# Kernel tuning notes

Hardware: AMD Instinct MI355X
Metric: run time of the kernel (lower is better)

## Reference

```python
import jax, jax.numpy as jnp
import numpy as np

DIM = 256
N = 262144
LN_EPS = 1e-5


def setup_inputs() -> dict:
    key = jax.random.key(0)
    ks = jax.random.split(key, 16)
    d = DIM
    inp = {
        "x": jax.random.normal(ks[0], (N, d), dtype=jnp.float32),
        # main cell params (torch Linear stores weight as [out, in])
        "W_slow": jax.random.normal(ks[1], (d, d), dtype=jnp.float32) / np.sqrt(d),
        "V_slow": jax.random.normal(ks[2], (d, d), dtype=jnp.float32) * (0.1 / np.sqrt(d)),
        "gate_w": jax.random.normal(ks[3], (1, d), dtype=jnp.float32) / np.sqrt(d),
        "gate_b": jnp.zeros((1,), dtype=jnp.float32),
        # homeostatic core: Linear(4,16) -> LN(16) -> Tanh -> Linear(16,8) -> ReLU -> Linear(8,4) -> Sigmoid
        "sens1_w": jax.random.normal(ks[4], (16, 4), dtype=jnp.float32) * 0.5,
        "sens1_b": jnp.zeros((16,), dtype=jnp.float32),
        "ln_g": jnp.ones((16,), dtype=jnp.float32),
        "ln_b": jnp.zeros((16,), dtype=jnp.float32),
        "sens2_w": jax.random.normal(ks[5], (8, 16), dtype=jnp.float32) * 0.25,
        "sens2_b": jnp.zeros((8,), dtype=jnp.float32),
        "act_w": jax.random.normal(ks[6], (4, 8), dtype=jnp.float32) * 0.35,
        "act_b": jnp.zeros((4,), dtype=jnp.float32),
        # persistent Hebbian memory buffer
        "semantic_memory": jax.random.normal(ks[7], (d, d), dtype=jnp.float32) * 0.01,
    }
    return inp


def _homeostatic_controls(x, h_raw, w_norm, sens1_w, sens1_b, ln_g, ln_b,
                          sens2_w, sens2_b, act_w, act_b):
    # state vector: [surprise, excitation, fatigue, coherence]  -> [N, 4]
    surprise = jnp.abs(jnp.var(x, axis=1) - 0.5)          # unbiased=False variance
    excitation = jnp.mean(jnp.abs(h_raw), axis=1)
    fatigue = jnp.full_like(surprise, w_norm)
    coherence = jnp.full_like(surprise, 0.5)              # loss_val is None
    state = jnp.stack([surprise, excitation, fatigue, coherence], axis=1)
    z = state @ sens1_w.T + sens1_b                        # [N,16]
    mu = jnp.mean(z, axis=-1, keepdims=True)
    var = jnp.mean((z - mu) ** 2, axis=-1, keepdims=True)
    z = (z - mu) * jax.lax.rsqrt(var + LN_EPS) * ln_g + ln_b
    z = jnp.tanh(z)
    z = jax.nn.relu(z @ sens2_w.T + sens2_b)               # [N,8]
    controls = jax.nn.sigmoid(z @ act_w.T + act_b)         # [N,4]
    return controls


def reference(x, W_slow, V_slow, gate_w, gate_b,
              sens1_w, sens1_b, ln_g, ln_b, sens2_w, sens2_b, act_w, act_b,
              semantic_memory):
    # v = clamp(V_slow(x), -2, 2)
    v = jnp.clip(x @ V_slow.T, -2.0, 2.0)                  # [N, d]

    # homeostatic core (no_grad in torch)
    h_raw = x @ W_slow.T
    w_norm = jnp.linalg.norm(W_slow)
    controls = _homeostatic_controls(x, h_raw, w_norm, sens1_w, sens1_b,
                                     ln_g, ln_b, sens2_w, sens2_b, act_w, act_b)
    metabolic_rate = jnp.mean(controls[:, 0])
    gate_value = jnp.mean(controls[:, 2])

    gate = jax.nn.sigmoid(v @ gate_w.T + gate_b) * gate_value  # [N,1]
    output = jnp.clip(gate * v, -2.0, 2.0)

    # training-mode Hebbian memory update (no_grad in torch)
    batch = x.shape[0]
    hebb = (v.T @ x) / batch                               # [d, d]
    forget = jnp.mean(v ** 2, axis=0)[:, None] * semantic_memory
    delta = jnp.tanh(hebb - forget)
    mem = semantic_memory + delta * metabolic_rate * 0.1
    mem_norm = jnp.maximum(jnp.linalg.norm(mem), 1e-6)
    new_memory = mem / mem_norm * 0.5

    return output, new_memory
```

## Files before the change

### kernel.cpp

```cpp
#include <hip/hip_runtime.h>
#include <hip/hip_bf16.h>


#define NTOK 262144

typedef short s16x4 __attribute__((ext_vector_type(4)));
typedef short s16x8 __attribute__((ext_vector_type(8)));
typedef float f32x4 __attribute__((ext_vector_type(4)));
typedef unsigned int u32x4 __attribute__((ext_vector_type(4)));
typedef __bf16 bf16x8 __attribute__((ext_vector_type(8)));

static __device__ __forceinline__ float b2f(short s) {
  unsigned int u = ((unsigned int)(unsigned short)s) << 16;
  return __builtin_bit_cast(float, u);
}
static __device__ __forceinline__ short f2b(float f) {
  __hip_bfloat16 h = __float2bfloat16(f);
  return (short)__builtin_bit_cast(unsigned short, h);
}
static __device__ __forceinline__ float clip2(float f) {
  return fminf(2.f, fmaxf(-2.f, f));
}
static __device__ __forceinline__ unsigned int packu(short lo, short hi) {
  return (unsigned int)(unsigned short)lo | ((unsigned int)(unsigned short)hi << 16);
}
static __device__ __forceinline__ f32x4 mfma16(s16x8 a, s16x8 b, f32x4 c) {
  return __builtin_amdgcn_mfma_f32_16x16x32_bf16(
      __builtin_bit_cast(bf16x8, a), __builtin_bit_cast(bf16x8, b), c, 0, 0, 0);
}

__global__ __launch_bounds__(1024) void k_prep(const float* __restrict__ V,
                                               const float* __restrict__ W,
                                               short* __restrict__ Vf,
                                               short* __restrict__ Wf,
                                               float* __restrict__ scal) {
  int t = blockIdx.x * 1024 + threadIdx.x;
  int flat = t * 4;
  int col = flat >> 8, k0 = flat & 255;
  f32x4 v4 = *(const f32x4*)(V + flat);
  f32x4 w4 = *(const f32x4*)(W + flat);
  s16x4 vb, wb;
  float s = 0.f;
#pragma unroll
  for (int e = 0; e < 4; ++e) {
    vb[e] = f2b(v4[e]);
    wb[e] = f2b(w4[e]);
    s += w4[e] * w4[e];
  }
  int cb = col >> 4, lrr = col & 15;
  int ks = k0 >> 5, lgg = (k0 >> 3) & 3, j0 = k0 & 7;
  size_t g = (size_t)(((cb * 8 + ks) * 4 + lgg) * 16 + lrr) * 8 + j0;
  *(s16x4*)(Vf + g) = vb;
  *(s16x4*)(Wf + g) = wb;
#pragma unroll
  for (int d = 1; d < 64; d <<= 1) s += __shfl_xor(s, d);
  __shared__ float r[16];
  if ((threadIdx.x & 63) == 0) r[threadIdx.x >> 6] = s;
  __syncthreads();
  if (threadIdx.x == 0) {
    float tt = 0.f;
#pragma unroll
    for (int i = 0; i < 16; ++i) tt += r[i];
    atomicAdd(&scal[0], tt);
  }
}

__global__ __launch_bounds__(512) void k_main(
    const float* __restrict__ x, const short* __restrict__ Vf,
    const short* __restrict__ Wf, const float* __restrict__ gw,
    const float* __restrict__ gb, const float* __restrict__ s1w,
    const float* __restrict__ s1b, const float* __restrict__ lng,
    const float* __restrict__ lnb, const float* __restrict__ s2w,
    const float* __restrict__ s2b, const float* __restrict__ aw,
    const float* __restrict__ ab, short* __restrict__ v_out,
    float* __restrict__ g_out, float* __restrict__ scal) {
  __shared__ __align__(16) short xs[1024 * 8];
  __shared__ __align__(16) short vs[32 * 264];
  __shared__ float stat[4096];
  int tid = threadIdx.x;
  int lane = tid & 63, wid = tid >> 6;
  int lr = lane & 15, lg = lane >> 4;
  int np = tid >> 5, ic = tid & 31;
  int c0 = wid * 32;
  size_t n0 = (size_t)blockIdx.x * 1024;

#pragma unroll
  for (int q = 0; q < 4; ++q) stat[q * 512 + tid] = 0.f;

  float gw0 = gw[c0 + lr], gw1 = gw[c0 + 16 + lr];
  int sks = ic >> 2, slg = ic & 3;

  for (int nt = 0; nt < 32; ++nt) {
    int rbase = nt * 32;
    if (nt > 0) {
#pragma unroll
      for (int q = 0; q < 2; ++q) {
        int item = q * 512 + tid;
        int row = item >> 5, c8 = item & 31;
        *(s16x8*)(v_out + (n0 + rbase - 32 + row) * 256 + c8 * 8) =
            *(const s16x8*)(vs + row * 264 + c8 * 8);
      }
    }
    {
      const float* pa = x + (n0 + rbase + 2 * np) * 256 + ic * 8;
      f32x4 xa0 = *(const f32x4*)pa;
      f32x4 xa1 = *(const f32x4*)(pa + 4);
      f32x4 xb0 = *(const f32x4*)(pa + 256);
      f32x4 xb1 = *(const f32x4*)(pa + 260);
      s16x8 ca, cb;
      float sA = 0.f, qA = 0.f, sB = 0.f, qB = 0.f;
#pragma unroll
      for (int j = 0; j < 4; ++j) {
        sA += xa0[j] + xa1[j];
        qA += xa0[j] * xa0[j] + xa1[j] * xa1[j];
        sB += xb0[j] + xb1[j];
        qB += xb0[j] * xb0[j] + xb1[j] * xb1[j];
        ca[j] = f2b(xa0[j]); ca[4 + j] = f2b(xa1[j]);
        cb[j] = f2b(xb0[j]); cb[4 + j] = f2b(xb1[j]);
      }
      int rowa = 2 * np, rowb = 2 * np + 1;
      int sa = ((rowa >> 4) * 8 + sks) * 64 + ((slg * 16 + (rowa & 15)) ^ sks);
      int sb = ((rowb >> 4) * 8 + sks) * 64 + ((slg * 16 + (rowb & 15)) ^ sks);
      *(s16x8*)(xs + sa * 8) = ca;
      *(s16x8*)(xs + sb * 8) = cb;
#pragma unroll
      for (int d = 1; d < 32; d <<= 1) {
        sA += __shfl_xor(sA, d); qA += __shfl_xor(qA, d);
        sB += __shfl_xor(sB, d); qB += __shfl_xor(qB, d);
      }
      if (ic == 0) {
        stat[2048 + rbase + 2 * np] = sA;
        stat[3072 + rbase + 2 * np] = qA;
        stat[2048 + rbase + 2 * np + 1] = sB;
        stat[3072 + rbase + 2 * np + 1] = qB;
      }
    }
    __syncthreads();
    f32x4 av[2][2] = {}, ah[2][2] = {};
#pragma unroll
    for (int ks = 0; ks < 8; ++ks) {
      s16x8 a0 = *(const s16x8*)(xs + ((ks * 64) + (lane ^ ks)) * 8);
      s16x8 a1 = *(const s16x8*)(xs + (((8 + ks) * 64) + (lane ^ ks)) * 8);
      s16x8 bv0 = *(const s16x8*)(Vf + (size_t)(((wid * 2 + 0) * 8 + ks) * 64 + lane) * 8);
      s16x8 bv1 = *(const s16x8*)(Vf + (size_t)(((wid * 2 + 1) * 8 + ks) * 64 + lane) * 8);
      s16x8 bw0 = *(const s16x8*)(Wf + (size_t)(((wid * 2 + 0) * 8 + ks) * 64 + lane) * 8);
      s16x8 bw1 = *(const s16x8*)(Wf + (size_t)(((wid * 2 + 1) * 8 + ks) * 64 + lane) * 8);
      av[0][0] = mfma16(a0, bv0, av[0][0]);
      av[0][1] = mfma16(a0, bv1, av[0][1]);
      av[1][0] = mfma16(a1, bv0, av[1][0]);
      av[1][1] = mfma16(a1, bv1, av[1][1]);
      ah[0][0] = mfma16(a0, bw0, ah[0][0]);
      ah[0][1] = mfma16(a0, bw1, ah[0][1]);
      ah[1][0] = mfma16(a1, bw0, ah[1][0]);
      ah[1][1] = mfma16(a1, bw1, ah[1][1]);
    }
#pragma unroll
    for (int mf = 0; mf < 2; ++mf)
#pragma unroll
      for (int e = 0; e < 4; ++e) {
        float v0 = clip2(av[mf][0][e]), v1 = clip2(av[mf][1][e]);
        av[mf][0][e] = v0; av[mf][1][e] = v1;
        float gd = v0 * gw0 + v1 * gw1;
        float hs = fabsf(ah[mf][0][e]) + fabsf(ah[mf][1][e]);
#pragma unroll
        for (int d = 1; d < 16; d <<= 1) {
          gd += __shfl_xor(gd, d);
          hs += __shfl_xor(hs, d);
        }
        if (lr == 0) {
          int row = rbase + mf * 16 + lg * 4 + e;
          atomicAdd(&stat[row], gd);
          atomicAdd(&stat[1024 + row], hs);
        }
      }
#pragma unroll
    for (int mf = 0; mf < 2; ++mf)
#pragma unroll
      for (int nf = 0; nf < 2; ++nf)
#pragma unroll
        for (int e = 0; e < 4; ++e)
          vs[(mf * 16 + lg * 4 + e) * 264 + c0 + nf * 16 + lr] =
              f2b(av[mf][nf][e]);
    __syncthreads();
  }
#pragma unroll
  for (int q = 0; q < 2; ++q) {
    int item = q * 512 + tid;
    int row = item >> 5, c8 = item & 31;
    *(s16x8*)(v_out + (n0 + 992 + row) * 256 + c8 * 8) =
        *(const s16x8*)(vs + row * 264 + c8 * 8);
  }

  float c0s = 0.f, c2s = 0.f;
  float wnorm = sqrtf(scal[0]);
#pragma unroll
  for (int rr = 0; rr < 2; ++rr) {
    int r = tid + rr * 512;
    float mean = stat[2048 + r] * (1.f / 256.f);
    float var = stat[3072 + r] * (1.f / 256.f) - mean * mean;
    float st[4];
    st[0] = fabsf(var - 0.5f);
    st[1] = stat[1024 + r] * (1.f / 256.f);
    st[2] = wnorm;
    st[3] = 0.5f;
    float z[16];
#pragma unroll
    for (int o = 0; o < 16; ++o) {
      float a = s1b[o];
#pragma unroll
      for (int i = 0; i < 4; ++i) a += s1w[o * 4 + i] * st[i];
      z[o] = a;
    }
    float mu = 0.f;
#pragma unroll
    for (int o = 0; o < 16; ++o) mu += z[o];
    mu *= (1.f / 16.f);
    float vz = 0.f;
#pragma unroll
    for (int o = 0; o < 16; ++o) { float d2 = z[o] - mu; vz += d2 * d2; }
    vz *= (1.f / 16.f);
    float rs = rsqrtf(vz + 1e-5f);
#pragma unroll
    for (int o = 0; o < 16; ++o)
      z[o] = tanhf((z[o] - mu) * rs * lng[o] + lnb[o]);
    float z2[8];
#pragma unroll
    for (int o = 0; o < 8; ++o) {
      float a = s2b[o];
#pragma unroll
      for (int i = 0; i < 16; ++i) a += s2w[o * 16 + i] * z[i];
      z2[o] = fmaxf(a, 0.f);
    }
#pragma unroll
    for (int q = 0; q < 2; ++q) {
      int o = q * 2;
      float a = ab[o];
#pragma unroll
      for (int i = 0; i < 8; ++i) a += aw[o * 8 + i] * z2[i];
      float cc = 1.f / (1.f + expf(-a));
      if (q == 0) c0s += cc; else c2s += cc;
    }
    g_out[n0 + r] = 1.f / (1.f + expf(-(stat[r] + gb[0])));
  }
#pragma unroll
  for (int d = 1; d < 64; d <<= 1) {
    c0s += __shfl_xor(c0s, d);
    c2s += __shfl_xor(c2s, d);
  }
  if (lane == 0) {
    atomicAdd(&scal[1], c0s);
    atomicAdd(&scal[2], c2s);
  }
}

__global__ __launch_bounds__(512, 2) void k_hebb(
    const float* __restrict__ x, const short* __restrict__ v_in,
    const float* __restrict__ g_sig, const float* __restrict__ scal,
    float* __restrict__ colv2, float* __restrict__ parts,
    float* __restrict__ out0) {
  __shared__ __align__(16) unsigned int ldsT[2 * 256 * 17];
  unsigned int* vT = ldsT;
  unsigned int* xT = ldsT + 256 * 17;
  int tid = threadIdx.x;
  int lane = tid & 63, wid = tid >> 6;
  int lr = lane & 15, lg = lane >> 4;
  int wr = wid >> 2, wc = wid & 3;
  size_t n0 = (size_t)blockIdx.x * 1024;
  float gv = scal[2] * (1.f / 262144.f);

  f32x4 acc[8][4] = {};
  float cv2[8] = {0.f, 0.f, 0.f, 0.f, 0.f, 0.f, 0.f, 0.f};
  int np = tid >> 5, ic = tid & 31, i0 = ic * 8;

  for (int nt = 0; nt < 32; ++nt) {
    size_t nr = n0 + nt * 32 + np * 2;
    s16x8 va = *(const s16x8*)(v_in + nr * 256 + i0);
    s16x8 vb = *(const s16x8*)(v_in + (nr + 1) * 256 + i0);
    f32x4 xa0 = *(const f32x4*)(x + nr * 256 + i0);
    f32x4 xa1 = *(const f32x4*)(x + nr * 256 + i0 + 4);
    f32x4 xb0 = *(const f32x4*)(x + (nr + 1) * 256 + i0);
    f32x4 xb1 = *(const f32x4*)(x + (nr + 1) * 256 + i0 + 4);
    float sa = g_sig[nr] * gv, sb = g_sig[nr + 1] * gv;
    f32x4 oa0, oa1, ob0, ob1;
#pragma unroll
    for (int j = 0; j < 4; ++j) {
      float fa = b2f(va[j]), fA = b2f(va[4 + j]);
      float fb = b2f(vb[j]), fB = b2f(vb[4 + j]);
      cv2[j] += fa * fa + fb * fb;
      cv2[4 + j] += fA * fA + fB * fB;
      oa0[j] = clip2(fa * sa); oa1[j] = clip2(fA * sa);
      ob0[j] = clip2(fb * sb); ob1[j] = clip2(fB * sb);
      vT[(i0 + j) * 17 + np] = packu(va[j], vb[j]);
      vT[(i0 + 4 + j) * 17 + np] = packu(va[4 + j], vb[4 + j]);
      xT[(i0 + j) * 17 + np] = packu(f2b(xa0[j]), f2b(xb0[j]));
      xT[(i0 + 4 + j) * 17 + np] = packu(f2b(xa1[j]), f2b(xb1[j]));
    }
    *(f32x4*)(out0 + nr * 256 + i0) = oa0;
    *(f32x4*)(out0 + nr * 256 + i0 + 4) = oa1;
    *(f32x4*)(out0 + (nr + 1) * 256 + i0) = ob0;
    *(f32x4*)(out0 + (nr + 1) * 256 + i0 + 4) = ob1;
    __syncthreads();
    int npb = lg * 4;
    s16x8 bfr[4];
#pragma unroll
    for (int nf = 0; nf < 4; ++nf) {
      int j = wc * 64 + nf * 16 + lr;
      u32x4 q;
      q[0] = xT[j * 17 + npb]; q[1] = xT[j * 17 + npb + 1];
      q[2] = xT[j * 17 + npb + 2]; q[3] = xT[j * 17 + npb + 3];
      bfr[nf] = __builtin_bit_cast(s16x8, q);
    }
#pragma unroll
    for (int mf = 0; mf < 8; ++mf) {
      int i = wr * 128 + mf * 16 + lr;
      u32x4 q;
      q[0] = vT[i * 17 + npb]; q[1] = vT[i * 17 + npb + 1];
      q[2] = vT[i * 17 + npb + 2]; q[3] = vT[i * 17 + npb + 3];
      s16x8 afr = __builtin_bit_cast(s16x8, q);
#pragma unroll
      for (int nf = 0; nf < 4; ++nf)
        acc[mf][nf] = mfma16(afr, bfr[nf], acc[mf][nf]);
    }
    __syncthreads();
  }
  float* myp = parts + (size_t)blockIdx.x * 65536;
#pragma unroll
  for (int mf = 0; mf < 8; ++mf)
#pragma unroll
    for (int nf = 0; nf < 4; ++nf)
      *(f32x4*)(myp + (size_t)(((wid * 8 + mf) * 4 + nf) * 64 + lane) * 4) =
          acc[mf][nf];
  __syncthreads();
  float* cred = (float*)ldsT;
  if (tid < 256) cred[tid] = 0.f;
  __syncthreads();
#pragma unroll
  for (int j = 0; j < 8; ++j) atomicAdd(&cred[i0 + j], cv2[j]);
  __syncthreads();
  if (tid < 256) atomicAdd(&colv2[tid], cred[tid]);
}

__global__ __launch_bounds__(256) void k_mem1(
    const float* __restrict__ parts, const float* __restrict__ colv2,
    const float* __restrict__ sm, float* __restrict__ mem,
    float* __restrict__ scal) {
  int q = blockIdx.x * 256 + threadIdx.x;
  const float* src = parts + (size_t)q * 4;
  f32x4 acc = {0.f, 0.f, 0.f, 0.f};
#pragma unroll 4
  for (int p = 0; p < 256; ++p) acc += *(const f32x4*)(src + (size_t)p * 65536);
  int lane2 = q & 63, r = q >> 6;
  int lg = lane2 >> 4, lr = lane2 & 15;
  int nf = r & 3, mf = (r >> 2) & 7, wid = r >> 5;
  int wr = wid >> 2, wc = wid & 3;
  int j = wc * 64 + nf * 16 + lr;
  float mr = scal[1] * (1.f / 262144.f);
  float s = 0.f;
#pragma unroll
  for (int e = 0; e < 4; ++e) {
    int i = wr * 128 + mf * 16 + lg * 4 + e;
    float hebb = acc[e] * (1.f / 262144.f);
    float smv = sm[i * 256 + j];
    float forget = colv2[i] * (1.f / 262144.f) * smv;
    float m = smv + tanhf(hebb - forget) * mr * 0.1f;
    mem[i * 256 + j] = m;
    s += m * m;
  }
#pragma unroll
  for (int d = 1; d < 64; d <<= 1) s += __shfl_xor(s, d);
  __shared__ float r4[4];
  if ((threadIdx.x & 63) == 0) r4[threadIdx.x >> 6] = s;
  __syncthreads();
  if (threadIdx.x == 0) atomicAdd(&scal[3], r4[0] + r4[1] + r4[2] + r4[3]);
}

__global__ __launch_bounds__(256) void k_mem2(const float* __restrict__ mem,
                                              const float* __restrict__ scal,
                                              float* __restrict__ out1) {
  int idx = blockIdx.x * 256 + threadIdx.x;
  float scale = 0.5f / fmaxf(sqrtf(scal[3]), 1e-6f);
  out1[idx] = mem[idx] * scale;
}

extern "C" void kernel_launch(void* const* d_in, const int* in_sizes, int n_in,
                              void* d_out, int out_size, void* d_ws, size_t ws_size,
                              hipStream_t stream) {
  (void)in_sizes; (void)n_in; (void)out_size; (void)ws_size;
  const float* x   = (const float*)d_in[0];
  const float* Wm  = (const float*)d_in[1];
  const float* Vm  = (const float*)d_in[2];
  const float* gw  = (const float*)d_in[3];
  const float* gb  = (const float*)d_in[4];
  const float* s1w = (const float*)d_in[5];
  const float* s1b = (const float*)d_in[6];
  const float* lng = (const float*)d_in[7];
  const float* lnb = (const float*)d_in[8];
  const float* s2w = (const float*)d_in[9];
  const float* s2b = (const float*)d_in[10];
  const float* aw  = (const float*)d_in[11];
  const float* ab  = (const float*)d_in[12];
  const float* sm  = (const float*)d_in[13];
  float* out0 = (float*)d_out;
  float* out1 = out0 + (size_t)NTOK * 256;

  char* w = (char*)d_ws;
  short* v_ws  = (short*)w;
  float* g_ws  = (float*)(w + 134217728);
  float* scal  = (float*)(w + 135266304);
  float* colv2 = (float*)(w + 135266560);
  float* mem   = (float*)(w + 135267584);
  float* parts = (float*)(w + 135529728);
  short* Vf    = (short*)(w + 202638592);
  short* Wf    = (short*)(w + 202769664);

  hipMemsetAsync(scal, 0, 1280, stream);
  k_prep<<<16, 1024, 0, stream>>>(Vm, Wm, Vf, Wf, scal);
  k_main<<<256, 512, 0, stream>>>(x, Vf, Wf, gw, gb, s1w, s1b, lng, lnb,
                                  s2w, s2b, aw, ab, v_ws, g_ws, scal);
  k_hebb<<<256, 512, 0, stream>>>(x, v_ws, g_ws, scal, colv2, parts, out0);
  k_mem1<<<64, 256, 0, stream>>>(parts, colv2, sm, mem, scal);
  k_mem2<<<256, 256, 0, stream>>>(mem, scal, out1);
}
```

Before: 388.7 us.

## Double-buffer x tile and v staging in k_main to overlap loads with MFMA

Double-buffers the x-tile and v-staging shared-memory buffers in the main kernel. The next tile's x global loads are issued into registers before the MFMA loop and converted and stored to the alternate buffer afterward. This removes one __syncthreads per iteration and hides global-load latency behind compute. In exchange it roughly doubles the LDS footprint and raises register pressure, which may reduce occupancy.

```diff
diff --git a/kernel.cpp b/kernel.cpp
--- a/kernel.cpp
+++ b/kernel.cpp
@@ -74,8 +74,8 @@
     const float* __restrict__ s2b, const float* __restrict__ aw,
     const float* __restrict__ ab, short* __restrict__ v_out,
     float* __restrict__ g_out, float* __restrict__ scal) {
-  __shared__ __align__(16) short xs[1024 * 8];
-  __shared__ __align__(16) short vs[32 * 264];
+  __shared__ __align__(16) short xs[2][8192];
+  __shared__ __align__(16) short vs[2][32 * 264];
   __shared__ float stat[4096];
   int tid = threadIdx.x;
   int lane = tid & 63, wid = tid >> 6;
@@ -89,58 +89,70 @@
 
   float gw0 = gw[c0 + lr], gw1 = gw[c0 + 16 + lr];
   int sks = ic >> 2, slg = ic & 3;
+  int rowa = 2 * np, rowb = 2 * np + 1;
+  int sa = ((rowa >> 4) * 8 + sks) * 64 + ((slg * 16 + (rowa & 15)) ^ sks);
+  int sb = ((rowb >> 4) * 8 + sks) * 64 + ((slg * 16 + (rowb & 15)) ^ sks);
+
+  f32x4 rxa0, rxa1, rxb0, rxb1;
+
+#define XLOAD(RB)                                              \
+  {                                                            \
+    const float* pa = x + (n0 + (RB) + rowa) * 256 + ic * 8;   \
+    rxa0 = *(const f32x4*)pa;                                  \
+    rxa1 = *(const f32x4*)(pa + 4);                            \
+    rxb0 = *(const f32x4*)(pa + 256);                          \
+    rxb1 = *(const f32x4*)(pa + 260);                          \
+  }
+#define CONV_STORE(BUF, RB)                                    \
+  {                                                            \
+    s16x8 ca, cb;                                              \
+    float sA = 0.f, qA = 0.f, sB = 0.f, qB = 0.f;              \
+    _Pragma("unroll") for (int j = 0; j < 4; ++j) {            \
+      sA += rxa0[j] + rxa1[j];                                 \
+      qA += rxa0[j] * rxa0[j] + rxa1[j] * rxa1[j];             \
+      sB += rxb0[j] + rxb1[j];                                 \
+      qB += rxb0[j] * rxb0[j] + rxb1[j] * rxb1[j];             \
+      ca[j] = f2b(rxa0[j]); ca[4 + j] = f2b(rxa1[j]);          \
+      cb[j] = f2b(rxb0[j]); cb[4 + j] = f2b(rxb1[j]);          \
+    }                                                          \
+    *(s16x8*)(xs[BUF] + sa * 8) = ca;                          \
+    *(s16x8*)(xs[BUF] + sb * 8) = cb;                          \
+    _Pragma("unroll") for (int d = 1; d < 32; d <<= 1) {       \
+      sA += __shfl_xor(sA, d); qA += __shfl_xor(qA, d);        \
+      sB += __shfl_xor(sB, d); qB += __shfl_xor(qB, d);        \
+    }                                                          \
+    if (ic == 0) {                                             \
+      stat[2048 + (RB) + rowa] = sA;                           \
+      stat[3072 + (RB) + rowa] = qA;                           \
+      stat[2048 + (RB) + rowb] = sB;                           \
+      stat[3072 + (RB) + rowb] = qB;                           \
+    }                                                          \
+  }
+
+  XLOAD(0);
+  CONV_STORE(0, 0);
+  __syncthreads();
 
   for (int nt = 0; nt < 32; ++nt) {
+    int buf = nt & 1;
     int rbase = nt * 32;
     if (nt > 0) {
+      const short* vsp = vs[buf ^ 1];
 #pragma unroll
       for (int q = 0; q < 2; ++q) {
         int item = q * 512 + tid;
         int row = item >> 5, c8 = item & 31;
         *(s16x8*)(v_out + (n0 + rbase - 32 + row) * 256 + c8 * 8) =
-            *(const s16x8*)(vs + row * 264 + c8 * 8);
+            *(const s16x8*)(vsp + row * 264 + c8 * 8);
       }
     }
-    {
-      const float* pa = x + (n0 + rbase + 2 * np) * 256 + ic * 8;
-      f32x4 xa0 = *(const f32x4*)pa;
-      f32x4 xa1 = *(const f32x4*)(pa + 4);
-      f32x4 xb0 = *(const f32x4*)(pa + 256);
-      f32x4 xb1 = *(const f32x4*)(pa + 260);
-      s16x8 ca, cb;
-      float sA = 0.f, qA = 0.f, sB = 0.f, qB = 0.f;
-#pragma unroll
-      for (int j = 0; j < 4; ++j) {
-        sA += xa0[j] + xa1[j];
-        qA += xa0[j] * xa0[j] + xa1[j] * xa1[j];
-        sB += xb0[j] + xb1[j];
-        qB += xb0[j] * xb0[j] + xb1[j] * xb1[j];
-        ca[j] = f2b(xa0[j]); ca[4 + j] = f2b(xa1[j]);
-        cb[j] = f2b(xb0[j]); cb[4 + j] = f2b(xb1[j]);
-      }
-      int rowa = 2 * np, rowb = 2 * np + 1;
-      int sa = ((rowa >> 4) * 8 + sks) * 64 + ((slg * 16 + (rowa & 15)) ^ sks);
-      int sb = ((rowb >> 4) * 8 + sks) * 64 + ((slg * 16 + (rowb & 15)) ^ sks);
-      *(s16x8*)(xs + sa * 8) = ca;
-      *(s16x8*)(xs + sb * 8) = cb;
-#pragma unroll
-      for (int d = 1; d < 32; d <<= 1) {
-        sA += __shfl_xor(sA, d); qA += __shfl_xor(qA, d);
-        sB += __shfl_xor(sB, d); qB += __shfl_xor(qB, d);
-      }
-      if (ic == 0) {
-        stat[2048 + rbase + 2 * np] = sA;
-        stat[3072 + rbase + 2 * np] = qA;
-        stat[2048 + rbase + 2 * np + 1] = sB;
-        stat[3072 + rbase + 2 * np + 1] = qB;
-      }
-    }
-    __syncthreads();
+    if (nt < 31) XLOAD(rbase + 32);
     f32x4 av[2][2] = {}, ah[2][2] = {};
+    const short* xb = xs[buf];
 #pragma unroll
     for (int ks = 0; ks < 8; ++ks) {
-      s16x8 a0 = *(const s16x8*)(xs + ((ks * 64) + (lane ^ ks)) * 8);
-      s16x8 a1 = *(const s16x8*)(xs + (((8 + ks) * 64) + (lane ^ ks)) * 8);
+      s16x8 a0 = *(const s16x8*)(xb + ((ks * 64) + (lane ^ ks)) * 8);
+      s16x8 a1 = *(const s16x8*)(xb + (((8 + ks) * 64) + (lane ^ ks)) * 8);
       s16x8 bv0 = *(const s16x8*)(Vf + (size_t)(((wid * 2 + 0) * 8 + ks) * 64 + lane) * 8);
       s16x8 bv1 = *(const s16x8*)(Vf + (size_t)(((wid * 2 + 1) * 8 + ks) * 64 + lane) * 8);
       s16x8 bw0 = *(const s16x8*)(Wf + (size_t)(((wid * 2 + 0) * 8 + ks) * 64 + lane) * 8);
@@ -173,23 +185,32 @@
           atomicAdd(&stat[1024 + row], hs);
         }
       }
-#pragma unroll
-    for (int mf = 0; mf < 2; ++mf)
-#pragma unroll
-      for (int nf = 0; nf < 2; ++nf)
-#pragma unroll
-        for (int e = 0; e < 4; ++e)
-          vs[(mf * 16 + lg * 4 + e) * 264 + c0 + nf * 16 + lr] =
-              f2b(av[mf][nf][e]);
+    {
+      short* vsc = vs[buf];
+#pragma unroll
+      for (int mf = 0; mf < 2; ++mf)
+#pragma unroll
+        for (int nf = 0; nf < 2; ++nf)
+#pragma unroll
+          for (int e = 0; e < 4; ++e)
+            vsc[(mf * 16 + lg * 4 + e) * 264 + c0 + nf * 16 + lr] =
+                f2b(av[mf][nf][e]);
+    }
+    if (nt < 31) CONV_STORE(buf ^ 1, rbase + 32);
     __syncthreads();
   }
-#pragma unroll
-  for (int q = 0; q < 2; ++q) {
-    int item = q * 512 + tid;
-    int row = item >> 5, c8 = item & 31;
-    *(s16x8*)(v_out + (n0 + 992 + row) * 256 + c8 * 8) =
-        *(const s16x8*)(vs + row * 264 + c8 * 8);
-  }
+  {
+    const short* vsp = vs[1];
+#pragma unroll
+    for (int q = 0; q < 2; ++q) {
+      int item = q * 512 + tid;
+      int row = item >> 5, c8 = item & 31;
+      *(s16x8*)(v_out + (n0 + 992 + row) * 256 + c8 * 8) =
+          *(const s16x8*)(vsp + row * 264 + c8 * 8);
+    }
+  }
+#undef CONV_STORE
+#undef XLOAD
 
   float c0s = 0.f, c2s = 0.f;
   float wnorm = sqrtf(scal[0]);
```

New measurement: 370.7 us. 1.05x faster.
